# Kernel optimization log

Measured on AMD Instinct MI355X. Metric: run time of the kernel, lower is better.

Reference implementation:

```python
import jax, jax.numpy as jnp
import numpy as np

T, D, E, K, F, SF = 4096, 1024, 8, 2, 1024, 1024  # tokens, d_model, experts, top_k, moe_ff, shared_ff


def setup_inputs() -> dict:
    key = jax.random.key(0)
    ks = jax.random.split(key, 10)
    hidden_states = jax.random.normal(ks[0], (T, D), jnp.float32)
    # balanced expert assignment: the fused kernel's get_split_sizes assumes tokens
    # split evenly across experts after permute_tokens, so exactly T*K/E per expert
    flat = jnp.arange(T * K) % E
    flat = jax.random.permutation(ks[1], flat)
    topk_indices = flat.reshape(T, K).astype(jnp.int32)
    w = jax.random.uniform(ks[2], (T, K), jnp.float32)
    topk_weights = w / w.sum(-1, keepdims=True)  # norm_topk_prob
    s = 0.02
    w_gate = jax.random.normal(ks[3], (E, D, F), jnp.float32) * s
    w_up = jax.random.normal(ks[4], (E, D, F), jnp.float32) * s
    w_down = jax.random.normal(ks[5], (E, F, D), jnp.float32) * s
    sw_gate = jax.random.normal(ks[6], (D, SF), jnp.float32) * s
    sw_up = jax.random.normal(ks[7], (D, SF), jnp.float32) * s
    sw_down = jax.random.normal(ks[8], (SF, D), jnp.float32) * s
    shared_gate_w = jax.random.normal(ks[9], (D, 1), jnp.float32) * s
    return dict(hidden_states=hidden_states, topk_weights=topk_weights,
                w_gate=w_gate, w_up=w_up, w_down=w_down,
                sw_gate=sw_gate, sw_up=sw_up, sw_down=sw_down,
                shared_gate_w=shared_gate_w, topk_indices=topk_indices)


def _silu(x):
    return x * jax.nn.sigmoid(x)


def reference(hidden_states, topk_weights, w_gate, w_up, w_down,
              sw_gate, sw_up, sw_down, shared_gate_w, topk_indices):
    t, d = hidden_states.shape
    e = w_gate.shape[0]
    k = topk_indices.shape[1]
    c = (t * k) // e  # tokens per expert (balanced split, as in get_split_sizes)

    # permute_tokens: replicate each token top_k times and sort by expert id
    flat_idx = topk_indices.reshape(-1)                    # [t*k]
    order = jnp.argsort(flat_idx)                          # dispatch permutation
    x_rep = jnp.repeat(hidden_states, k, axis=0)           # [t*k, d]
    xs = x_rep[order].reshape(e, c, d)                     # grouped per-expert

    # per-expert gated MLP (grouped GEMMs)
    h = _silu(jnp.einsum('ecd,edf->ecf', xs, w_gate)) * jnp.einsum('ecd,edf->ecf', xs, w_up)
    y = jnp.einsum('ecf,efd->ecd', h, w_down).reshape(t * k, d)

    # unpermute_tokens + weighted combine over top_k
    y = y[jnp.argsort(order)].reshape(t, k, d)
    out = (y * topk_weights[..., None]).sum(axis=1)        # [t, d]

    # shared expert with sigmoid gate
    s = jnp.einsum('tf,fd->td', _silu(hidden_states @ sw_gate) * (hidden_states @ sw_up), sw_down)
    g = jax.nn.sigmoid(hidden_states @ shared_gate_w)      # [t, 1]
    return (out + g * s).astype(hidden_states.dtype)
```

## Files before the change

kernel.cpp:

```cpp
#include <hip/hip_runtime.h>
#include <hip/hip_bf16.h>
#include <cstdint>
#include <cstddef>

#define TTOK 4096
#define DM   1024
#define NE   8
#define KTOP 2
#define FFD  1024
#define CPER 1024
#define MROWS 12288

typedef __attribute__((ext_vector_type(8))) short frag8;
typedef __attribute__((ext_vector_type(4))) float f32x4;

static __device__ __forceinline__ unsigned short f2bf(float f) {
  unsigned int u = __float_as_uint(f);
  u += 0x7fff + ((u >> 16) & 1);
  return (unsigned short)(u >> 16);
}
static __device__ __forceinline__ float bf2f(unsigned short u) {
  return __uint_as_float((unsigned int)u << 16);
}

static __device__ __forceinline__ void gld_lds16(const unsigned short* g, unsigned short* l) {
  __builtin_amdgcn_global_load_lds(
      (const __attribute__((address_space(1))) unsigned int*)g,
      (__attribute__((address_space(3))) unsigned int*)l,
      16, 0, 0);
}

static __device__ __forceinline__ int lds_slot64(int r, int c) {
  return r * 8 + (c ^ (r & 7));
}

static __device__ __forceinline__ void stage_tile64(const unsigned short* __restrict__ src,
                                                    int row0, int k0,
                                                    unsigned short* lds, int tid) {
#pragma unroll
  for (int it = 0; it < 4; ++it) {
    int seg = it * 256 + tid;
    int r = seg >> 3;
    int cs = (seg & 7) ^ (r & 7);
    gld_lds16(src + (size_t)(row0 + r) * 1024 + k0 + cs * 8, lds + seg * 8);
  }
}

static __device__ __forceinline__ void swizzle_xy(int& x, int& y) {
  int L = blockIdx.y * 8 + blockIdx.x;
  int xcd = L & 7;
  int s = L >> 3;
  y = xcd * 12 + s % 12;
  x = s / 12;
}

__global__ void prep_kernel(const float* __restrict__ x, const float* __restrict__ gw,
                            const int* __restrict__ idx, const float* __restrict__ tw,
                            int* __restrict__ cnt, int* __restrict__ rowsrc,
                            int* __restrict__ inv, float* __restrict__ rowscale,
                            unsigned short* __restrict__ xb) {
  if (blockIdx.x < 32) {
    int i = blockIdx.x * 256 + threadIdx.x;
    int e = idx[i];
    int pos = atomicAdd(&cnt[e], 1);
    int j = e * CPER + pos;
    rowsrc[j] = i >> 1;
    rowscale[j] = tw[i];
    inv[i] = j;
    if (i < TTOK) rowsrc[8192 + i] = i;
  }
  int row = blockIdx.x * 4 + (threadIdx.x >> 6);
  int lane = threadIdx.x & 63;
  const float4* xr = (const float4*)(x + (size_t)row * 1024);
  const float4* wr = (const float4*)gw;
  ushort4* ob = (ushort4*)(xb + (size_t)row * 1024);
  float s = 0.f;
#pragma unroll
  for (int c = 0; c < 4; ++c) {
    int k = lane + 64 * c;
    float4 v = xr[k];
    float4 g = wr[k];
    s += v.x * g.x + v.y * g.y + v.z * g.z + v.w * g.w;
    ushort4 o;
    o.x = f2bf(v.x); o.y = f2bf(v.y); o.z = f2bf(v.z); o.w = f2bf(v.w);
    ob[k] = o;
  }
#pragma unroll
  for (int off = 32; off; off >>= 1) s += __shfl_down(s, off);
  if (lane == 0) rowscale[8192 + row] = 1.f / (1.f + __expf(-s));
}

__global__ void transw_kernel(const float* __restrict__ wg, const float* __restrict__ wu,
                              const float* __restrict__ wd, const float* __restrict__ sg,
                              const float* __restrict__ su, const float* __restrict__ sd,
                              unsigned short* __restrict__ owg, unsigned short* __restrict__ owu,
                              unsigned short* __restrict__ owd) {
  int z = blockIdx.z;
  const float* src; unsigned short* dst;
  if (z < 8)       { src = wg + (size_t)z * 1048576;        dst = owg + (size_t)z * 1048576; }
  else if (z < 16) { src = wu + (size_t)(z - 8) * 1048576;  dst = owu + (size_t)(z - 8) * 1048576; }
  else if (z < 24) { src = wd + (size_t)(z - 16) * 1048576; dst = owd + (size_t)(z - 16) * 1048576; }
  else if (z == 24){ src = sg; dst = owg + (size_t)8 * 1048576; }
  else if (z == 25){ src = su; dst = owu + (size_t)8 * 1048576; }
  else             { src = sd; dst = owd + (size_t)8 * 1048576; }
  __shared__ float tile[64][65];
  int bx = blockIdx.x * 64;
  int by = blockIdx.y * 64;
  int c4 = threadIdx.x & 15;
  int r0 = threadIdx.x >> 4;
#pragma unroll
  for (int i = 0; i < 4; ++i) {
    int r = r0 + 16 * i;
    float4 v = *(const float4*)&src[(size_t)(by + r) * 1024 + bx + c4 * 4];
    tile[r][c4 * 4 + 0] = v.x; tile[r][c4 * 4 + 1] = v.y;
    tile[r][c4 * 4 + 2] = v.z; tile[r][c4 * 4 + 3] = v.w;
  }
  __syncthreads();
#pragma unroll
  for (int i = 0; i < 4; ++i) {
    int f = r0 + 16 * i;
    ushort4 o;
    o.x = f2bf(tile[c4 * 4 + 0][f]);
    o.y = f2bf(tile[c4 * 4 + 1][f]);
    o.z = f2bf(tile[c4 * 4 + 2][f]);
    o.w = f2bf(tile[c4 * 4 + 3][f]);
    *(ushort4*)&dst[(size_t)(bx + f) * 1024 + by + c4 * 4] = o;
  }
}

static __device__ __forceinline__ int eid_of(int y) { return (y < 64) ? (y >> 3) : 8; }

__global__ __launch_bounds__(256, 2) void gemm1_kernel(
    const unsigned short* __restrict__ A, const int* __restrict__ rowsrc,
    const unsigned short* __restrict__ Bg, const unsigned short* __restrict__ Bu,
    unsigned short* __restrict__ H) {
  __shared__ __align__(16) unsigned short As[128 * 64];
  __shared__ __align__(16) unsigned short Bgs[128 * 64];
  __shared__ __align__(16) unsigned short Bus[128 * 64];
  int tid = threadIdx.x;
  int bx, by;
  swizzle_xy(bx, by);
  int e = eid_of(by);
  int row0 = by * 128;
  int col0 = bx * 128;
  const unsigned short* Bge = Bg + (size_t)e * 1048576;
  const unsigned short* Bue = Bu + (size_t)e * 1048576;

  const unsigned short* pA[4];
#pragma unroll
  for (int it = 0; it < 4; ++it) {
    int seg = it * 256 + tid;
    int r = seg >> 3;
    int cs = (seg & 7) ^ (r & 7);
    pA[it] = A + (size_t)rowsrc[row0 + r] * 1024 + cs * 8;
  }

  int wave = tid >> 6, lane = tid & 63;
  int wm = wave >> 1, wn = wave & 1;
  int lr = lane & 15, q = lane >> 4;

  f32x4 accg[4][4], accu[4][4];
#pragma unroll
  for (int i = 0; i < 4; ++i)
#pragma unroll
    for (int j = 0; j < 4; ++j) {
      accg[i][j] = (f32x4){0.f, 0.f, 0.f, 0.f};
      accu[i][j] = (f32x4){0.f, 0.f, 0.f, 0.f};
    }

  for (int kt = 0; kt < 1024; kt += 64) {
#pragma unroll
    for (int it = 0; it < 4; ++it)
      gld_lds16(pA[it] + kt, As + (it * 256 + tid) * 8);
    stage_tile64(Bge, col0, kt, Bgs, tid);
    stage_tile64(Bue, col0, kt, Bus, tid);
    __syncthreads();
#pragma unroll
    for (int kk = 0; kk < 2; ++kk) {
      int c = kk * 4 + q;
      frag8 a[4], b0[4], b1[4];
#pragma unroll
      for (int i = 0; i < 4; ++i) {
        int r = wm * 64 + i * 16 + lr;
        a[i] = *(const frag8*)&As[lds_slot64(r, c) * 8];
      }
#pragma unroll
      for (int j = 0; j < 4; ++j) {
        int r = wn * 64 + j * 16 + lr;
        b0[j] = *(const frag8*)&Bgs[lds_slot64(r, c) * 8];
        b1[j] = *(const frag8*)&Bus[lds_slot64(r, c) * 8];
      }
#pragma unroll
      for (int i = 0; i < 4; ++i)
#pragma unroll
        for (int j = 0; j < 4; ++j) {
          accg[i][j] = __builtin_amdgcn_mfma_f32_16x16x32_bf16(a[i], b0[j], accg[i][j], 0, 0, 0);
          accu[i][j] = __builtin_amdgcn_mfma_f32_16x16x32_bf16(a[i], b1[j], accu[i][j], 0, 0, 0);
        }
    }
    __syncthreads();
  }
#pragma unroll
  for (int i = 0; i < 4; ++i)
#pragma unroll
    for (int j = 0; j < 4; ++j)
#pragma unroll
      for (int r = 0; r < 4; ++r) {
        int m = row0 + wm * 64 + i * 16 + q * 4 + r;
        int n = col0 + wn * 64 + j * 16 + lr;
        float gv = accg[i][j][r];
        float hv = gv / (1.f + __expf(-gv)) * accu[i][j][r];
        H[(size_t)m * 1024 + n] = f2bf(hv);
      }
}

__global__ __launch_bounds__(256, 2) void gemm2_kernel(
    const unsigned short* __restrict__ A, const unsigned short* __restrict__ B,
    const float* __restrict__ rowscale, unsigned short* __restrict__ Y) {
  __shared__ __align__(16) unsigned short As[128 * 64];
  __shared__ __align__(16) unsigned short Bs[128 * 64];
  int tid = threadIdx.x;
  int bx, by;
  swizzle_xy(bx, by);
  int e = eid_of(by);
  int row0 = by * 128;
  int col0 = bx * 128;
  const unsigned short* Be = B + (size_t)e * 1048576;

  int wave = tid >> 6, lane = tid & 63;
  int wm = wave >> 1, wn = wave & 1;
  int lr = lane & 15, q = lane >> 4;

  f32x4 acc[4][4];
#pragma unroll
  for (int i = 0; i < 4; ++i)
#pragma unroll
    for (int j = 0; j < 4; ++j) acc[i][j] = (f32x4){0.f, 0.f, 0.f, 0.f};

  for (int kt = 0; kt < 1024; kt += 64) {
    stage_tile64(A, row0, kt, As, tid);
    stage_tile64(Be, col0, kt, Bs, tid);
    __syncthreads();
#pragma unroll
    for (int kk = 0; kk < 2; ++kk) {
      int c = kk * 4 + q;
      frag8 a[4], b[4];
#pragma unroll
      for (int i = 0; i < 4; ++i) {
        int r = wm * 64 + i * 16 + lr;
        a[i] = *(const frag8*)&As[lds_slot64(r, c) * 8];
      }
#pragma unroll
      for (int j = 0; j < 4; ++j) {
        int r = wn * 64 + j * 16 + lr;
        b[j] = *(const frag8*)&Bs[lds_slot64(r, c) * 8];
      }
#pragma unroll
      for (int i = 0; i < 4; ++i)
#pragma unroll
        for (int j = 0; j < 4; ++j)
          acc[i][j] = __builtin_amdgcn_mfma_f32_16x16x32_bf16(a[i], b[j], acc[i][j], 0, 0, 0);
    }
    __syncthreads();
  }
#pragma unroll
  for (int i = 0; i < 4; ++i)
#pragma unroll
    for (int r = 0; r < 4; ++r) {
      int m = row0 + wm * 64 + i * 16 + q * 4 + r;
      float sc = rowscale[m];
#pragma unroll
      for (int j = 0; j < 4; ++j) {
        int n = col0 + wn * 64 + j * 16 + lr;
        Y[(size_t)m * 1024 + n] = f2bf(sc * acc[i][j][r]);
      }
    }
}

__global__ void combine_kernel(const unsigned short* __restrict__ Y,
                               const int* __restrict__ inv, float* __restrict__ out) {
  int base = blockIdx.x * 256 + threadIdx.x;
#pragma unroll
  for (int k = 0; k < 2; ++k) {
    int slot = base + k * 524288;
    int t = slot >> 8;
    int c = slot & 255;
    int j0 = inv[2 * t], j1 = inv[2 * t + 1];
    ushort4 a = ((const ushort4*)(Y + (size_t)j0 * 1024))[c];
    ushort4 b = ((const ushort4*)(Y + (size_t)j1 * 1024))[c];
    ushort4 s = ((const ushort4*)(Y + (size_t)(8192 + t) * 1024))[c];
    float4 o;
    o.x = bf2f(a.x) + bf2f(b.x) + bf2f(s.x);
    o.y = bf2f(a.y) + bf2f(b.y) + bf2f(s.y);
    o.z = bf2f(a.z) + bf2f(b.z) + bf2f(s.z);
    o.w = bf2f(a.w) + bf2f(b.w) + bf2f(s.w);
    ((float4*)(out + (size_t)t * 1024))[c] = o;
  }
}

extern "C" void kernel_launch(void* const* d_in, const int* in_sizes, int n_in,
                              void* d_out, int out_size, void* d_ws, size_t ws_size,
                              hipStream_t stream) {
  (void)in_sizes; (void)n_in; (void)out_size; (void)ws_size;
  const float* hidden  = (const float*)d_in[0];
  const float* topk_w  = (const float*)d_in[1];
  const float* w_gate  = (const float*)d_in[2];
  const float* w_up    = (const float*)d_in[3];
  const float* w_down  = (const float*)d_in[4];
  const float* sw_gate = (const float*)d_in[5];
  const float* sw_up   = (const float*)d_in[6];
  const float* sw_down = (const float*)d_in[7];
  const float* sgw     = (const float*)d_in[8];
  const int*   topk_i  = (const int*)d_in[9];
  float* out = (float*)d_out;

  char* p = (char*)d_ws;
  auto alloc = [&](size_t bytes) {
    char* r = p;
    p += (bytes + 255) & ~(size_t)255;
    return r;
  };
  unsigned short* Wg_all = (unsigned short*)alloc((size_t)9 * 1048576 * 2);
  unsigned short* Wu_all = (unsigned short*)alloc((size_t)9 * 1048576 * 2);
  unsigned short* Wd_all = (unsigned short*)alloc((size_t)9 * 1048576 * 2);
  unsigned short* Xbf    = (unsigned short*)alloc((size_t)TTOK * 1024 * 2);
  unsigned short* Hall   = (unsigned short*)alloc((size_t)MROWS * 1024 * 2);
  unsigned short* Yall   = (unsigned short*)alloc((size_t)MROWS * 1024 * 2);
  int*   cnt      = (int*)alloc(NE * 4);
  int*   rowsrc   = (int*)alloc((size_t)MROWS * 4);
  int*   inv      = (int*)alloc((size_t)TTOK * KTOP * 4);
  float* rowscale = (float*)alloc((size_t)MROWS * 4);

  hipMemsetAsync(cnt, 0, NE * 4, stream);

  prep_kernel<<<TTOK / 4, 256, 0, stream>>>(hidden, sgw, topk_i, topk_w,
                                            cnt, rowsrc, inv, rowscale, Xbf);
  transw_kernel<<<dim3(16, 16, 27), 256, 0, stream>>>(
      w_gate, w_up, w_down, sw_gate, sw_up, sw_down, Wg_all, Wu_all, Wd_all);

  gemm1_kernel<<<dim3(8, 96), 256, 0, stream>>>(Xbf, rowsrc, Wg_all, Wu_all, Hall);
  gemm2_kernel<<<dim3(8, 96), 256, 0, stream>>>(Hall, Wd_all, rowscale, Yall);
  combine_kernel<<<2048, 256, 0, stream>>>(Yall, inv, out);
}
```

Before: 297.7 us.

## Double-buffer LDS tiles with BK=32 and async prefetch in MoE GEMMs

Both grouped GEMM kernels now use two LDS buffers with a K-tile of 32 instead of one buffer with a K-tile of 64. The next tile is prefetched with direct global-to-LDS loads while MFMAs run on the current one, gated by explicit vmcnt waits and raw barriers. MFMA sections are wrapped in s_setprio raises. The change targets the load-then-compute stall of the single-buffer loop, at the cost of twice as many barrier points per K, and it relies on hand-counted vmcnt values that assume a fixed number of outstanding loads.

```diff
diff --git a/kernel.cpp b/kernel.cpp
--- a/kernel.cpp
+++ b/kernel.cpp
@@ -10,6 +10,7 @@
 #define FFD  1024
 #define CPER 1024
 #define MROWS 12288
+#define NT   32
 
 typedef __attribute__((ext_vector_type(8))) short frag8;
 typedef __attribute__((ext_vector_type(4))) float f32x4;
@@ -30,20 +31,8 @@
       16, 0, 0);
 }
 
-static __device__ __forceinline__ int lds_slot64(int r, int c) {
-  return r * 8 + (c ^ (r & 7));
-}
-
-static __device__ __forceinline__ void stage_tile64(const unsigned short* __restrict__ src,
-                                                    int row0, int k0,
-                                                    unsigned short* lds, int tid) {
-#pragma unroll
-  for (int it = 0; it < 4; ++it) {
-    int seg = it * 256 + tid;
-    int r = seg >> 3;
-    int cs = (seg & 7) ^ (r & 7);
-    gld_lds16(src + (size_t)(row0 + r) * 1024 + k0 + cs * 8, lds + seg * 8);
-  }
+static __device__ __forceinline__ int lds_slot32(int r, int c) {
+  return r * 4 + (c ^ ((r >> 1) & 3));
 }
 
 static __device__ __forceinline__ void swizzle_xy(int& x, int& y) {
@@ -134,9 +123,9 @@
     const unsigned short* __restrict__ A, const int* __restrict__ rowsrc,
     const unsigned short* __restrict__ Bg, const unsigned short* __restrict__ Bu,
     unsigned short* __restrict__ H) {
-  __shared__ __align__(16) unsigned short As[128 * 64];
-  __shared__ __align__(16) unsigned short Bgs[128 * 64];
-  __shared__ __align__(16) unsigned short Bus[128 * 64];
+  __shared__ __align__(16) unsigned short As[2][128 * 32];
+  __shared__ __align__(16) unsigned short Bgs[2][128 * 32];
+  __shared__ __align__(16) unsigned short Bus[2][128 * 32];
   int tid = threadIdx.x;
   int bx, by;
   swizzle_xy(bx, by);
@@ -146,13 +135,15 @@
   const unsigned short* Bge = Bg + (size_t)e * 1048576;
   const unsigned short* Bue = Bu + (size_t)e * 1048576;
 
-  const unsigned short* pA[4];
-#pragma unroll
-  for (int it = 0; it < 4; ++it) {
+  const unsigned short *pA[2], *pBg[2], *pBu[2];
+#pragma unroll
+  for (int it = 0; it < 2; ++it) {
     int seg = it * 256 + tid;
-    int r = seg >> 3;
-    int cs = (seg & 7) ^ (r & 7);
-    pA[it] = A + (size_t)rowsrc[row0 + r] * 1024 + cs * 8;
+    int r = seg >> 2;
+    int cs = (seg & 3) ^ ((r >> 1) & 3);
+    pA[it]  = A   + (size_t)rowsrc[row0 + r] * 1024 + cs * 8;
+    pBg[it] = Bge + (size_t)(col0 + r) * 1024 + cs * 8;
+    pBu[it] = Bue + (size_t)(col0 + r) * 1024 + cs * 8;
   }
 
   int wave = tid >> 6, lane = tid & 63;
@@ -168,37 +159,54 @@
       accu[i][j] = (f32x4){0.f, 0.f, 0.f, 0.f};
     }
 
-  for (int kt = 0; kt < 1024; kt += 64) {
-#pragma unroll
-    for (int it = 0; it < 4; ++it)
-      gld_lds16(pA[it] + kt, As + (it * 256 + tid) * 8);
-    stage_tile64(Bge, col0, kt, Bgs, tid);
-    stage_tile64(Bue, col0, kt, Bus, tid);
-    __syncthreads();
-#pragma unroll
-    for (int kk = 0; kk < 2; ++kk) {
-      int c = kk * 4 + q;
-      frag8 a[4], b0[4], b1[4];
-#pragma unroll
-      for (int i = 0; i < 4; ++i) {
-        int r = wm * 64 + i * 16 + lr;
-        a[i] = *(const frag8*)&As[lds_slot64(r, c) * 8];
-      }
+#pragma unroll
+  for (int it = 0; it < 2; ++it) {
+    int off = (it * 256 + tid) * 8;
+    gld_lds16(pA[it],  As[0] + off);
+    gld_lds16(pBg[it], Bgs[0] + off);
+    gld_lds16(pBu[it], Bus[0] + off);
+  }
+
+#pragma unroll 2
+  for (int t = 0; t < NT; ++t) {
+    int cur = t & 1;
+    if (t + 1 < NT) {
+      int kt = (t + 1) * 32;
+#pragma unroll
+      for (int it = 0; it < 2; ++it) {
+        int off = (it * 256 + tid) * 8;
+        gld_lds16(pA[it] + kt,  As[cur ^ 1] + off);
+        gld_lds16(pBg[it] + kt, Bgs[cur ^ 1] + off);
+        gld_lds16(pBu[it] + kt, Bus[cur ^ 1] + off);
+      }
+      asm volatile("s_waitcnt vmcnt(6)" ::: "memory");
+    } else {
+      asm volatile("s_waitcnt vmcnt(0)" ::: "memory");
+    }
+    __builtin_amdgcn_s_barrier();
+
+    frag8 a[4], b0[4], b1[4];
+#pragma unroll
+    for (int i = 0; i < 4; ++i) {
+      int r = wm * 64 + i * 16 + lr;
+      a[i] = *(const frag8*)&As[cur][lds_slot32(r, q) * 8];
+    }
+#pragma unroll
+    for (int j = 0; j < 4; ++j) {
+      int r = wn * 64 + j * 16 + lr;
+      b0[j] = *(const frag8*)&Bgs[cur][lds_slot32(r, q) * 8];
+      b1[j] = *(const frag8*)&Bus[cur][lds_slot32(r, q) * 8];
+    }
+    __builtin_amdgcn_s_setprio(1);
+#pragma unroll
+    for (int i = 0; i < 4; ++i)
 #pragma unroll
       for (int j = 0; j < 4; ++j) {
-        int r = wn * 64 + j * 16 + lr;
-        b0[j] = *(const frag8*)&Bgs[lds_slot64(r, c) * 8];
-        b1[j] = *(const frag8*)&Bus[lds_slot64(r, c) * 8];
-      }
-#pragma unroll
-      for (int i = 0; i < 4; ++i)
-#pragma unroll
-        for (int j = 0; j < 4; ++j) {
-          accg[i][j] = __builtin_amdgcn_mfma_f32_16x16x32_bf16(a[i], b0[j], accg[i][j], 0, 0, 0);
-          accu[i][j] = __builtin_amdgcn_mfma_f32_16x16x32_bf16(a[i], b1[j], accu[i][j], 0, 0, 0);
-        }
-    }
-    __syncthreads();
+        accg[i][j] = __builtin_amdgcn_mfma_f32_16x16x32_bf16(a[i], b0[j], accg[i][j], 0, 0, 0);
+        accu[i][j] = __builtin_amdgcn_mfma_f32_16x16x32_bf16(a[i], b1[j], accu[i][j], 0, 0, 0);
+      }
+    __builtin_amdgcn_s_setprio(0);
+    __builtin_amdgcn_s_barrier();
   }
 #pragma unroll
   for (int i = 0; i < 4; ++i)
@@ -217,8 +225,8 @@
 __global__ __launch_bounds__(256, 2) void gemm2_kernel(
     const unsigned short* __restrict__ A, const unsigned short* __restrict__ B,
     const float* __restrict__ rowscale, unsigned short* __restrict__ Y) {
-  __shared__ __align__(16) unsigned short As[128 * 64];
-  __shared__ __align__(16) unsigned short Bs[128 * 64];
+  __shared__ __align__(16) unsigned short As[2][128 * 32];
+  __shared__ __align__(16) unsigned short Bs[2][128 * 32];
   int tid = threadIdx.x;
   int bx, by;
   swizzle_xy(bx, by);
@@ -227,6 +235,16 @@
   int col0 = bx * 128;
   const unsigned short* Be = B + (size_t)e * 1048576;
 
+  const unsigned short *pA[2], *pB[2];
+#pragma unroll
+  for (int it = 0; it < 2; ++it) {
+    int seg = it * 256 + tid;
+    int r = seg >> 2;
+    int cs = (seg & 3) ^ ((r >> 1) & 3);
+    pA[it] = A  + (size_t)(row0 + r) * 1024 + cs * 8;
+    pB[it] = Be + (size_t)(col0 + r) * 1024 + cs * 8;
+  }
+
   int wave = tid >> 6, lane = tid & 63;
   int wm = wave >> 1, wn = wave & 1;
   int lr = lane & 15, q = lane >> 4;
@@ -237,31 +255,49 @@
 #pragma unroll
     for (int j = 0; j < 4; ++j) acc[i][j] = (f32x4){0.f, 0.f, 0.f, 0.f};
 
-  for (int kt = 0; kt < 1024; kt += 64) {
-    stage_tile64(A, row0, kt, As, tid);
-    stage_tile64(Be, col0, kt, Bs, tid);
-    __syncthreads();
-#pragma unroll
-    for (int kk = 0; kk < 2; ++kk) {
-      int c = kk * 4 + q;
-      frag8 a[4], b[4];
-#pragma unroll
-      for (int i = 0; i < 4; ++i) {
-        int r = wm * 64 + i * 16 + lr;
-        a[i] = *(const frag8*)&As[lds_slot64(r, c) * 8];
-      }
-#pragma unroll
-      for (int j = 0; j < 4; ++j) {
-        int r = wn * 64 + j * 16 + lr;
-        b[j] = *(const frag8*)&Bs[lds_slot64(r, c) * 8];
-      }
-#pragma unroll
-      for (int i = 0; i < 4; ++i)
-#pragma unroll
-        for (int j = 0; j < 4; ++j)
-          acc[i][j] = __builtin_amdgcn_mfma_f32_16x16x32_bf16(a[i], b[j], acc[i][j], 0, 0, 0);
-    }
-    __syncthreads();
+#pragma unroll
+  for (int it = 0; it < 2; ++it) {
+    int off = (it * 256 + tid) * 8;
+    gld_lds16(pA[it], As[0] + off);
+    gld_lds16(pB[it], Bs[0] + off);
+  }
+
+#pragma unroll 2
+  for (int t = 0; t < NT; ++t) {
+    int cur = t & 1;
+    if (t + 1 < NT) {
+      int kt = (t + 1) * 32;
+#pragma unroll
+      for (int it = 0; it < 2; ++it) {
+        int off = (it * 256 + tid) * 8;
+        gld_lds16(pA[it] + kt, As[cur ^ 1] + off);
+        gld_lds16(pB[it] + kt, Bs[cur ^ 1] + off);
+      }
+      asm volatile("s_waitcnt vmcnt(4)" ::: "memory");
+    } else {
+      asm volatile("s_waitcnt vmcnt(0)" ::: "memory");
+    }
+    __builtin_amdgcn_s_barrier();
+
+    frag8 a[4], b[4];
+#pragma unroll
+    for (int i = 0; i < 4; ++i) {
+      int r = wm * 64 + i * 16 + lr;
+      a[i] = *(const frag8*)&As[cur][lds_slot32(r, q) * 8];
+    }
+#pragma unroll
+    for (int j = 0; j < 4; ++j) {
+      int r = wn * 64 + j * 16 + lr;
+      b[j] = *(const frag8*)&Bs[cur][lds_slot32(r, q) * 8];
+    }
+    __builtin_amdgcn_s_setprio(1);
+#pragma unroll
+    for (int i = 0; i < 4; ++i)
+#pragma unroll
+      for (int j = 0; j < 4; ++j)
+        acc[i][j] = __builtin_amdgcn_mfma_f32_16x16x32_bf16(a[i], b[j], acc[i][j], 0, 0, 0);
+    __builtin_amdgcn_s_setprio(0);
+    __builtin_amdgcn_s_barrier();
   }
 #pragma unroll
   for (int i = 0; i < 4; ++i)
```

Measured after the change: 305.8 us. +2.7%, slower.
